# Kernel tuning notes

Measured on AMD Instinct MI355X. Metric: run time of the kernel, lower is better.

## Reference

```python
import jax, jax.numpy as jnp
import numpy as np

N = 100000
IN_C = 128
HID_C = 128
OUT_C = 128
E = 3200000


def setup_inputs() -> dict:
    key = jax.random.key(0)
    ks = jax.random.split(key, 8)
    x = jax.random.normal(ks[0], (N, IN_C), dtype=jnp.float32)
    edge_index = jax.random.randint(ks[1], (2, E), 0, N, dtype=jnp.int64)
    edge_weight = jnp.ones((E,), dtype=jnp.float32)
    s = 1.0 / np.sqrt(HID_C)
    W_conv = jax.random.uniform(ks[2], (HID_C, IN_C), jnp.float32, -s, s)
    b_conv = jnp.zeros((HID_C,), dtype=jnp.float32)
    W_fc = jax.random.uniform(ks[3], (HID_C, HID_C), jnp.float32, -s, s)
    b_fc = jax.random.uniform(ks[4], (HID_C,), jnp.float32, -s, s)
    W_fc2 = jax.random.uniform(ks[5], (OUT_C, HID_C), jnp.float32, -s, s)
    b_fc2 = jax.random.uniform(ks[6], (OUT_C,), jnp.float32, -s, s)
    return {"x": x, "edge_index": edge_index, "edge_weight": edge_weight,
            "W_conv": W_conv, "b_conv": b_conv, "W_fc": W_fc, "b_fc": b_fc,
            "W_fc2": W_fc2, "b_fc2": b_fc2}


def _gcn_conv(x, edge_index, edge_weight, W_conv, b_conv):
    n = x.shape[0]
    # add self-loops with weight 1 (PyG GCNConv default)
    loop = jnp.arange(n, dtype=edge_index.dtype)
    src = jnp.concatenate([edge_index[0], loop])
    dst = jnp.concatenate([edge_index[1], loop])
    ew = jnp.concatenate([edge_weight, jnp.ones((n,), dtype=edge_weight.dtype)])
    # symmetric normalization: deg^-1/2[src] * w * deg^-1/2[dst]
    deg = jax.ops.segment_sum(ew, dst, num_segments=n)
    dinv = jnp.where(deg > 0, jax.lax.rsqrt(jnp.where(deg > 0, deg, 1.0)), 0.0)
    norm = dinv[src] * ew * dinv[dst]  # [E+N]
    h = x @ W_conv.T                   # [N, hid], bias-free linear first
    msg = h[src] * norm[:, None]       # gather + scale
    agg = jax.ops.segment_sum(msg, dst, num_segments=n)  # scatter-add
    return agg + b_conv


def reference(x, edge_index, edge_weight, W_conv, b_conv, W_fc, b_fc, W_fc2, b_fc2):
    h = _gcn_conv(x, edge_index, edge_weight, W_conv, b_conv)
    h = jax.nn.relu(h)
    h = jax.nn.relu(h @ W_fc.T + b_fc)
    return h @ W_fc2.T + b_fc2
```

## Files before the change

kernel.cpp:

```cpp
#include <hip/hip_runtime.h>

typedef short bf16x8 __attribute__((ext_vector_type(8)));
typedef float f32x4 __attribute__((ext_vector_type(4)));

#define PS 64
#define PMAX 2048
#define CAPP 2432
#define NB 256

__device__ __forceinline__ unsigned short f2bf(float f) {
    unsigned int u = __float_as_uint(f);
    u = (u + 0x7FFFu + ((u >> 16) & 1u)) >> 16;
    return (unsigned short)u;
}
__device__ __forceinline__ float bf2f(unsigned short h) {
    return __uint_as_float(((unsigned int)h) << 16);
}

__global__ __launch_bounds__(1024) void scat_k(const int* __restrict__ ei,
                                               const float* __restrict__ ew,
                                               int* __restrict__ partCnt,
                                               int2* __restrict__ regions,
                                               int E, int P, int EPB) {
    __shared__ int cntl[PMAX];
    __shared__ int basel[PMAX];
    const int b = blockIdx.x, tid = threadIdx.x;
    for (int i = tid; i < P; i += 1024) cntl[i] = 0;
    __syncthreads();
    const int s = b * EPB, e = min(E, s + EPB);
    for (int i = s + tid; i < e; i += 1024)
        atomicAdd(&cntl[ei[E + i] >> 6], 1);
    __syncthreads();
    for (int p = tid; p < P; p += 1024) {
        int c = cntl[p];
        basel[p] = p * CAPP + (c ? atomicAdd(&partCnt[p], c) : 0);
        cntl[p] = 0;
    }
    __syncthreads();
    for (int i = s + tid; i < e; i += 1024) {
        int src = ei[i];
        int dst = ei[E + i];
        float w = ew[i];
        int p = dst >> 6, dl = dst & 63;
        int lidx = atomicAdd(&cntl[p], 1);
        int pos = basel[p] + lidx;
        if (pos < (p + 1) * CAPP)
            regions[pos] = make_int2(src | (dl << 24), __float_as_int(w));
    }
}

__global__ __launch_bounds__(256) void dgemm1_k(const float* __restrict__ x,
                                                const float* __restrict__ Wc,
                                                const int* __restrict__ partCnt,
                                                const int2* __restrict__ regions,
                                                float* __restrict__ dinv,
                                                unsigned short* __restrict__ h,
                                                int M, int P) {
    __shared__ __align__(16) unsigned short Wl[128 * 136];
    __shared__ float degl[256];
    const int tid = threadIdx.x;
    degl[tid] = 0.f;

#pragma unroll
    for (int i = 0; i < 16; ++i) {
        int e4 = i * 256 + tid;
        float4 v = ((const float4*)Wc)[e4];
        int e = e4 * 4, r = e >> 7, cc = e & 127;
        unsigned short* pp = &Wl[r * 136 + cc];
        pp[0] = f2bf(v.x); pp[1] = f2bf(v.y); pp[2] = f2bf(v.z); pp[3] = f2bf(v.w);
    }
    __syncthreads();

#pragma unroll
    for (int q = 0; q < 4; ++q) {
        int p = blockIdx.x * 4 + q;
        if (p < P) {
            const int cnt = min(partCnt[p], CAPP);
            const int2* reg = regions + (size_t)p * CAPP;
            for (int i = tid; i < cnt; i += 256) {
                int2 r = reg[i];
                atomicAdd(&degl[q * 64 + ((r.x >> 24) & 63)], __int_as_float(r.y));
            }
        }
    }
    __syncthreads();
    {
        int node = blockIdx.x * 256 + tid;
        float d = rsqrtf(1.0f + degl[tid]);
        if (node < M) dinv[node] = d;
        degl[tid] = d;
    }
    __syncthreads();

    const int wave = tid >> 6, lane = tid & 63;
    const int m = lane & 15, quad = lane >> 4;

#pragma unroll
    for (int t = 0; t < 4; ++t) {
        const int tileBase = blockIdx.x * 256 + t * 64;
        if (tileBase >= M) break;
        const int rowBase = tileBase + wave * 16;
        int arow = rowBase + m;
        int arowc = arow < M ? arow : (M - 1);

        bf16x8 afrag[4];
        const float* pa = x + (size_t)arowc * 128 + quad * 8;
#pragma unroll
        for (int kc = 0; kc < 4; ++kc) {
            float4 v0 = *(const float4*)(pa + kc * 32);
            float4 v1 = *(const float4*)(pa + kc * 32 + 4);
            bf16x8 f;
            f[0] = (short)f2bf(v0.x); f[1] = (short)f2bf(v0.y);
            f[2] = (short)f2bf(v0.z); f[3] = (short)f2bf(v0.w);
            f[4] = (short)f2bf(v1.x); f[5] = (short)f2bf(v1.y);
            f[6] = (short)f2bf(v1.z); f[7] = (short)f2bf(v1.w);
            afrag[kc] = f;
        }

        float dv[4];
#pragma unroll
        for (int r = 0; r < 4; ++r)
            dv[r] = degl[t * 64 + wave * 16 + quad * 4 + r];

#pragma unroll
        for (int nt = 0; nt < 8; ++nt) {
            f32x4 acc = {0.f, 0.f, 0.f, 0.f};
            const unsigned short* wb = &Wl[(nt * 16 + m) * 136 + quad * 8];
#pragma unroll
            for (int kc = 0; kc < 4; ++kc) {
                bf16x8 bfrag = *(const bf16x8*)(wb + kc * 32);
                acc = __builtin_amdgcn_mfma_f32_16x16x32_bf16(afrag[kc], bfrag, acc, 0, 0, 0);
            }
            const int col = nt * 16 + m;
#pragma unroll
            for (int r = 0; r < 4; ++r) {
                int row = rowBase + quad * 4 + r;
                if (row < M)
                    h[(size_t)row * 128 + col] = f2bf(acc[r] * dv[r]);
            }
        }
    }
}

__global__ __launch_bounds__(256) void aggF_k(const int* __restrict__ partCnt,
                                              const int2* __restrict__ regions,
                                              const unsigned short* __restrict__ h,
                                              const float* __restrict__ dinv,
                                              const float* __restrict__ bconv,
                                              unsigned short* __restrict__ h2, int N) {
    __shared__ __align__(16) int2 stag[CAPP];
    __shared__ int cl[PS];
    __shared__ int cstart[PS + 1];
    __shared__ int wcur[PS];
    const int p = blockIdx.x, tid = threadIdx.x;
    const int cnt = min(partCnt[p], CAPP);
    const int2* reg = regions + (size_t)p * CAPP;

    if (tid < PS) cl[tid] = 0;
    __syncthreads();
    for (int i = tid; i < cnt; i += 256)
        atomicAdd(&cl[(reg[i].x >> 24) & 63], 1);
    __syncthreads();
    if (tid < PS) {
        int cn = cl[tid];
        int v = cn;
#pragma unroll
        for (int off = 1; off < 64; off <<= 1) {
            int u = __shfl_up(v, off, 64);
            if (tid >= off) v += u;
        }
        cstart[tid + 1] = v;
        wcur[tid] = v - cn;
        if (tid == 0) cstart[0] = 0;
    }
    __syncthreads();
    for (int i = tid; i < cnt; i += 256) {
        int2 r = reg[i];
        int pos = atomicAdd(&wcur[(r.x >> 24) & 63], 1);
        stag[pos] = r;
    }
    __syncthreads();

    const int wave = tid >> 6, lane = tid & 63;
    const int g = lane >> 4;
    const int c8 = (lane & 15) * 8;
    for (int nl = wave; nl < PS; nl += 4) {
        int n = p * PS + nl;
        if (n >= N) continue;
        const int s = cstart[nl], e = cstart[nl + 1];
        float acc[8] = {0.f, 0.f, 0.f, 0.f, 0.f, 0.f, 0.f, 0.f};
        int j = s;
        const int efull = s + ((e - s) & ~15);
        for (; j < efull; j += 16) {
            int2 r0 = stag[j + g];
            int2 r1 = stag[j + 4 + g];
            int2 r2 = stag[j + 8 + g];
            int2 r3 = stag[j + 12 + g];
            float w0 = __int_as_float(r0.y), w1 = __int_as_float(r1.y);
            float w2 = __int_as_float(r2.y), w3 = __int_as_float(r3.y);
            int4 q0 = *(const int4*)(h + (((unsigned)r0.x & 0xFFFFFFu) << 7) + c8);
            int4 q1 = *(const int4*)(h + (((unsigned)r1.x & 0xFFFFFFu) << 7) + c8);
            int4 q2 = *(const int4*)(h + (((unsigned)r2.x & 0xFFFFFFu) << 7) + c8);
            int4 q3 = *(const int4*)(h + (((unsigned)r3.x & 0xFFFFFFu) << 7) + c8);
#pragma unroll
            for (int d = 0; d < 4; ++d) {
                unsigned ud = ((const unsigned*)&q0)[d];
                acc[2 * d]     += __uint_as_float(ud << 16) * w0;
                acc[2 * d + 1] += __uint_as_float(ud & 0xFFFF0000u) * w0;
            }
#pragma unroll
            for (int d = 0; d < 4; ++d) {
                unsigned ud = ((const unsigned*)&q1)[d];
                acc[2 * d]     += __uint_as_float(ud << 16) * w1;
                acc[2 * d + 1] += __uint_as_float(ud & 0xFFFF0000u) * w1;
            }
#pragma unroll
            for (int d = 0; d < 4; ++d) {
                unsigned ud = ((const unsigned*)&q2)[d];
                acc[2 * d]     += __uint_as_float(ud << 16) * w2;
                acc[2 * d + 1] += __uint_as_float(ud & 0xFFFF0000u) * w2;
            }
#pragma unroll
            for (int d = 0; d < 4; ++d) {
                unsigned ud = ((const unsigned*)&q3)[d];
                acc[2 * d]     += __uint_as_float(ud << 16) * w3;
                acc[2 * d + 1] += __uint_as_float(ud & 0xFFFF0000u) * w3;
            }
        }
        for (; j < e; j += 8) {
            int j0 = j + g, j1 = j + 4 + g;
            int2 r0 = stag[j0 < e ? j0 : s];
            int2 r1 = stag[j1 < e ? j1 : s];
            float w0 = (j0 < e) ? __int_as_float(r0.y) : 0.f;
            float w1 = (j1 < e) ? __int_as_float(r1.y) : 0.f;
            int4 q0 = *(const int4*)(h + (((unsigned)r0.x & 0xFFFFFFu) << 7) + c8);
            int4 q1 = *(const int4*)(h + (((unsigned)r1.x & 0xFFFFFFu) << 7) + c8);
#pragma unroll
            for (int d = 0; d < 4; ++d) {
                unsigned ud = ((const unsigned*)&q0)[d];
                acc[2 * d]     += __uint_as_float(ud << 16) * w0;
                acc[2 * d + 1] += __uint_as_float(ud & 0xFFFF0000u) * w0;
            }
#pragma unroll
            for (int d = 0; d < 4; ++d) {
                unsigned ud = ((const unsigned*)&q1)[d];
                acc[2 * d]     += __uint_as_float(ud << 16) * w1;
                acc[2 * d + 1] += __uint_as_float(ud & 0xFFFF0000u) * w1;
            }
        }
#pragma unroll
        for (int k = 0; k < 8; ++k) {
            float v = acc[k];
            v += __shfl_xor(v, 16, 64);
            v += __shfl_xor(v, 32, 64);
            acc[k] = v;
        }
        if (g == 0) {
            float di = dinv[n];
            int4 qs = *(const int4*)(h + ((unsigned)n << 7) + c8);
            float4 b0 = *(const float4*)(bconv + c8);
            float4 b1 = *(const float4*)(bconv + c8 + 4);
            float bb[8] = {b0.x, b0.y, b0.z, b0.w, b1.x, b1.y, b1.z, b1.w};
            bf16x8 o;
#pragma unroll
            for (int d = 0; d < 4; ++d) {
                unsigned ud = ((const unsigned*)&qs)[d];
                float h0 = __uint_as_float(ud << 16);
                float h1 = __uint_as_float(ud & 0xFFFF0000u);
                o[2 * d]     = (short)f2bf(fmaxf(di * (acc[2 * d] + h0) + bb[2 * d], 0.f));
                o[2 * d + 1] = (short)f2bf(fmaxf(di * (acc[2 * d + 1] + h1) + bb[2 * d + 1], 0.f));
            }
            *(bf16x8*)(h2 + (size_t)n * 128 + c8) = o;
        }
    }
}

__global__ __launch_bounds__(256) void gemm23_k(const unsigned short* __restrict__ h2,
                                                const float* __restrict__ Wf,
                                                const float* __restrict__ bfc,
                                                const float* __restrict__ W2,
                                                const float* __restrict__ b2,
                                                float* __restrict__ out, int M) {
    __shared__ __align__(16) unsigned short Wl[128 * 136];
    __shared__ __align__(16) unsigned short Tl[64 * 136];
    const int tid = threadIdx.x;

#pragma unroll
    for (int i = 0; i < 16; ++i) {
        int e4 = i * 256 + tid;
        float4 v = ((const float4*)Wf)[e4];
        int e = e4 * 4, r = e >> 7, cc = e & 127;
        unsigned short* pp = &Wl[r * 136 + cc];
        pp[0] = f2bf(v.x); pp[1] = f2bf(v.y); pp[2] = f2bf(v.z); pp[3] = f2bf(v.w);
    }
    __syncthreads();

    const int wave = tid >> 6, lane = tid & 63;
    const int m = lane & 15, quad = lane >> 4;
    const int rowBase = blockIdx.x * 64 + wave * 16;
    int arow = rowBase + m;
    int arowc = arow < M ? arow : (M - 1);

    bf16x8 afrag[4];
    {
        const unsigned short* pa = h2 + (size_t)arowc * 128 + quad * 8;
#pragma unroll
        for (int kc = 0; kc < 4; ++kc)
            afrag[kc] = *(const bf16x8*)(pa + kc * 32);
    }

#pragma unroll
    for (int nt = 0; nt < 8; ++nt) {
        f32x4 acc = {0.f, 0.f, 0.f, 0.f};
        const unsigned short* wb = &Wl[(nt * 16 + m) * 136 + quad * 8];
#pragma unroll
        for (int kc = 0; kc < 4; ++kc) {
            bf16x8 bfrag = *(const bf16x8*)(wb + kc * 32);
            acc = __builtin_amdgcn_mfma_f32_16x16x32_bf16(afrag[kc], bfrag, acc, 0, 0, 0);
        }
        const int col = nt * 16 + m;
        float bv = bfc[col];
#pragma unroll
        for (int r = 0; r < 4; ++r) {
            int rowl = wave * 16 + quad * 4 + r;
            Tl[rowl * 136 + col] = f2bf(fmaxf(acc[r] + bv, 0.f));
        }
    }
    __syncthreads();

#pragma unroll
    for (int i = 0; i < 16; ++i) {
        int e4 = i * 256 + tid;
        float4 v = ((const float4*)W2)[e4];
        int e = e4 * 4, r = e >> 7, cc = e & 127;
        unsigned short* pp = &Wl[r * 136 + cc];
        pp[0] = f2bf(v.x); pp[1] = f2bf(v.y); pp[2] = f2bf(v.z); pp[3] = f2bf(v.w);
    }
    __syncthreads();

    bf16x8 afrag2[4];
    {
        const unsigned short* pa = &Tl[(wave * 16 + m) * 136 + quad * 8];
#pragma unroll
        for (int kc = 0; kc < 4; ++kc)
            afrag2[kc] = *(const bf16x8*)(pa + kc * 32);
    }
#pragma unroll
    for (int nt = 0; nt < 8; ++nt) {
        f32x4 acc = {0.f, 0.f, 0.f, 0.f};
        const unsigned short* wb = &Wl[(nt * 16 + m) * 136 + quad * 8];
#pragma unroll
        for (int kc = 0; kc < 4; ++kc) {
            bf16x8 bfrag = *(const bf16x8*)(wb + kc * 32);
            acc = __builtin_amdgcn_mfma_f32_16x16x32_bf16(afrag2[kc], bfrag, acc, 0, 0, 0);
        }
        const int col = nt * 16 + m;
        float bv = b2[col];
#pragma unroll
        for (int r = 0; r < 4; ++r) {
            int row = rowBase + quad * 4 + r;
            if (row < M)
                out[(size_t)row * 128 + col] = acc[r] + bv;
        }
    }
}

extern "C" void kernel_launch(void* const* d_in, const int* in_sizes, int n_in,
                              void* d_out, int out_size, void* d_ws, size_t ws_size,
                              hipStream_t stream) {
    const float* x  = (const float*)d_in[0];
    const int* ei   = (const int*)d_in[1];
    const float* ew = (const float*)d_in[2];
    const float* Wc = (const float*)d_in[3];
    const float* bc = (const float*)d_in[4];
    const float* Wf = (const float*)d_in[5];
    const float* bf = (const float*)d_in[6];
    const float* W2 = (const float*)d_in[7];
    const float* b2 = (const float*)d_in[8];
    float* out = (float*)d_out;

    const int N = in_sizes[0] / 128;
    const int E = in_sizes[2];
    const int P = (N + PS - 1) / PS;

    auto align256 = [](size_t v) { return (v + 255) & ~(size_t)255; };
    char* ws = (char*)d_ws;
    size_t off = 0;
    float* dinv  = (float*)(ws + off); off += align256((size_t)N * 4);
    int* partCnt = (int*)(ws + off);   off += align256((size_t)P * 4);
    unsigned short* h  = (unsigned short*)(ws + off); off += (size_t)N * 256;
    unsigned short* h2 = (unsigned short*)(ws + off);

    int2* regions = (int2*)out;

    const int EPB = (E + NB - 1) / NB;

    hipMemsetAsync(partCnt, 0, (size_t)P * 4, stream);
    scat_k<<<NB, 1024, 0, stream>>>(ei, ew, partCnt, regions, E, P, EPB);
    dgemm1_k<<<(N + 255) / 256, 256, 0, stream>>>(x, Wc, partCnt, regions, dinv, h, N, P);
    aggF_k<<<P, 256, 0, stream>>>(partCnt, regions, h, dinv, bc, h2, N);
    gemm23_k<<<(N + 63) / 64, 256, 0, stream>>>(h2, Wf, bf, W2, b2, out, N);
}
```

Baseline: 384.2 us.

## Pre-convert weights to bf16, cache edge data in LDS, precompute node offsets, pipeline gathers

Adds a prologue kernel that converts all three weight matrices to bf16 once and zeroes the partition counters, replacing the memset. The GEMM kernels then read bf16 weights straight from global memory instead of staging converted copies in LDS. scat_k keeps dst and weight in LDS between its two passes so they are not reloaded from global memory. dgemm1_k now computes per-node offsets within each partition, which lets aggF_k skip its counting pass. aggF_k's gather loop is software-pipelined, prefetching the next 16 edges while the current chunk is accumulated. In exchange, scat_k uses about 100KB of LDS and may run at lower occupancy, and MFMA B operands now come from global or L2 rather than LDS.

```diff
diff --git a/kernel.cpp b/kernel.cpp
--- a/kernel.cpp
+++ b/kernel.cpp
@@ -7,14 +7,25 @@
 #define PMAX 2048
 #define CAPP 2432
 #define NB 256
+#define EPBC 12544
 
 __device__ __forceinline__ unsigned short f2bf(float f) {
     unsigned int u = __float_as_uint(f);
     u = (u + 0x7FFFu + ((u >> 16) & 1u)) >> 16;
     return (unsigned short)u;
 }
-__device__ __forceinline__ float bf2f(unsigned short h) {
-    return __uint_as_float(((unsigned int)h) << 16);
+
+__global__ __launch_bounds__(256) void pre_k(const float* __restrict__ Wc,
+                                             const float* __restrict__ Wf,
+                                             const float* __restrict__ W2,
+                                             unsigned short* __restrict__ Wb,
+                                             int* __restrict__ partCnt, int P) {
+    int i = blockIdx.x * 256 + threadIdx.x;
+    if (i < 3 * 16384) {
+        const float* src = (i < 16384) ? Wc : (i < 32768 ? Wf : W2);
+        Wb[i] = f2bf(src[i & 16383]);
+    }
+    if (i < P) partCnt[i] = 0;
 }
 
 __global__ __launch_bounds__(1024) void scat_k(const int* __restrict__ ei,
@@ -24,12 +35,19 @@
                                                int E, int P, int EPB) {
     __shared__ int cntl[PMAX];
     __shared__ int basel[PMAX];
+    __shared__ int dstl[EPBC];
+    __shared__ float ewl[EPBC];
     const int b = blockIdx.x, tid = threadIdx.x;
+    const bool useL = (EPB <= EPBC);
     for (int i = tid; i < P; i += 1024) cntl[i] = 0;
     __syncthreads();
     const int s = b * EPB, e = min(E, s + EPB);
-    for (int i = s + tid; i < e; i += 1024)
-        atomicAdd(&cntl[ei[E + i] >> 6], 1);
+    for (int i = s + tid; i < e; i += 1024) {
+        int dst = ei[E + i];
+        float w = ew[i];
+        if (useL) { dstl[i - s] = dst; ewl[i - s] = w; }
+        atomicAdd(&cntl[dst >> 6], 1);
+    }
     __syncthreads();
     for (int p = tid; p < P; p += 1024) {
         int c = cntl[p];
@@ -39,8 +57,8 @@
     __syncthreads();
     for (int i = s + tid; i < e; i += 1024) {
         int src = ei[i];
-        int dst = ei[E + i];
-        float w = ew[i];
+        int dst = useL ? dstl[i - s] : ei[E + i];
+        float w = useL ? ewl[i - s] : ew[i];
         int p = dst >> 6, dl = dst & 63;
         int lidx = atomicAdd(&cntl[p], 1);
         int pos = basel[p] + lidx;
@@ -50,25 +68,17 @@
 }
 
 __global__ __launch_bounds__(256) void dgemm1_k(const float* __restrict__ x,
-                                                const float* __restrict__ Wc,
+                                                const unsigned short* __restrict__ Wcb,
                                                 const int* __restrict__ partCnt,
                                                 const int2* __restrict__ regions,
                                                 float* __restrict__ dinv,
+                                                int* __restrict__ nodeOff,
                                                 unsigned short* __restrict__ h,
                                                 int M, int P) {
-    __shared__ __align__(16) unsigned short Wl[128 * 136];
     __shared__ float degl[256];
+    __shared__ int cl[256];
     const int tid = threadIdx.x;
-    degl[tid] = 0.f;
-
-#pragma unroll
-    for (int i = 0; i < 16; ++i) {
-        int e4 = i * 256 + tid;
-        float4 v = ((const float4*)Wc)[e4];
-        int e = e4 * 4, r = e >> 7, cc = e & 127;
-        unsigned short* pp = &Wl[r * 136 + cc];
-        pp[0] = f2bf(v.x); pp[1] = f2bf(v.y); pp[2] = f2bf(v.z); pp[3] = f2bf(v.w);
-    }
+    degl[tid] = 0.f; cl[tid] = 0;
     __syncthreads();
 
 #pragma unroll
@@ -79,15 +89,25 @@
             const int2* reg = regions + (size_t)p * CAPP;
             for (int i = tid; i < cnt; i += 256) {
                 int2 r = reg[i];
-                atomicAdd(&degl[q * 64 + ((r.x >> 24) & 63)], __int_as_float(r.y));
+                int dl = q * 64 + ((r.x >> 24) & 63);
+                atomicAdd(&cl[dl], 1);
+                atomicAdd(&degl[dl], __int_as_float(r.y));
             }
         }
     }
     __syncthreads();
     {
+        int lane = tid & 63;
+        int cn = cl[tid];
+        int v = cn;
+#pragma unroll
+        for (int off = 1; off < 64; off <<= 1) {
+            int u = __shfl_up(v, off, 64);
+            if (lane >= off) v += u;
+        }
         int node = blockIdx.x * 256 + tid;
         float d = rsqrtf(1.0f + degl[tid]);
-        if (node < M) dinv[node] = d;
+        if (node < M) { nodeOff[node] = v - cn; dinv[node] = d; }
         degl[tid] = d;
     }
     __syncthreads();
@@ -125,10 +145,9 @@
 #pragma unroll
         for (int nt = 0; nt < 8; ++nt) {
             f32x4 acc = {0.f, 0.f, 0.f, 0.f};
-            const unsigned short* wb = &Wl[(nt * 16 + m) * 136 + quad * 8];
 #pragma unroll
             for (int kc = 0; kc < 4; ++kc) {
-                bf16x8 bfrag = *(const bf16x8*)(wb + kc * 32);
+                bf16x8 bfrag = *(const bf16x8*)(Wcb + (nt * 16 + m) * 128 + kc * 32 + quad * 8);
                 acc = __builtin_amdgcn_mfma_f32_16x16x32_bf16(afrag[kc], bfrag, acc, 0, 0, 0);
             }
             const int col = nt * 16 + m;
@@ -143,35 +162,26 @@
 }
 
 __global__ __launch_bounds__(256) void aggF_k(const int* __restrict__ partCnt,
+                                              const int* __restrict__ nodeOff,
                                               const int2* __restrict__ regions,
                                               const unsigned short* __restrict__ h,
                                               const float* __restrict__ dinv,
                                               const float* __restrict__ bconv,
                                               unsigned short* __restrict__ h2, int N) {
     __shared__ __align__(16) int2 stag[CAPP];
-    __shared__ int cl[PS];
     __shared__ int cstart[PS + 1];
     __shared__ int wcur[PS];
     const int p = blockIdx.x, tid = threadIdx.x;
     const int cnt = min(partCnt[p], CAPP);
     const int2* reg = regions + (size_t)p * CAPP;
 
-    if (tid < PS) cl[tid] = 0;
-    __syncthreads();
-    for (int i = tid; i < cnt; i += 256)
-        atomicAdd(&cl[(reg[i].x >> 24) & 63], 1);
-    __syncthreads();
     if (tid < PS) {
-        int cn = cl[tid];
-        int v = cn;
-#pragma unroll
-        for (int off = 1; off < 64; off <<= 1) {
-            int u = __shfl_up(v, off, 64);
-            if (tid >= off) v += u;
-        }
-        cstart[tid + 1] = v;
-        wcur[tid] = v - cn;
-        if (tid == 0) cstart[0] = 0;
+        int node = p * PS + tid;
+        int o = (node < N) ? nodeOff[node] : cnt;
+        cstart[tid] = o;
+        wcur[tid] = o;
+    } else if (tid == PS) {
+        cstart[PS] = cnt;
     }
     __syncthreads();
     for (int i = tid; i < cnt; i += 256) {
@@ -187,67 +197,58 @@
     for (int nl = wave; nl < PS; nl += 4) {
         int n = p * PS + nl;
         if (n >= N) continue;
-        const int s = cstart[nl], e = cstart[nl + 1];
+        const int s0 = cstart[nl], e0 = cstart[nl + 1];
         float acc[8] = {0.f, 0.f, 0.f, 0.f, 0.f, 0.f, 0.f, 0.f};
-        int j = s;
-        const int efull = s + ((e - s) & ~15);
-        for (; j < efull; j += 16) {
-            int2 r0 = stag[j + g];
-            int2 r1 = stag[j + 4 + g];
-            int2 r2 = stag[j + 8 + g];
-            int2 r3 = stag[j + 12 + g];
-            float w0 = __int_as_float(r0.y), w1 = __int_as_float(r1.y);
-            float w2 = __int_as_float(r2.y), w3 = __int_as_float(r3.y);
-            int4 q0 = *(const int4*)(h + (((unsigned)r0.x & 0xFFFFFFu) << 7) + c8);
-            int4 q1 = *(const int4*)(h + (((unsigned)r1.x & 0xFFFFFFu) << 7) + c8);
-            int4 q2 = *(const int4*)(h + (((unsigned)r2.x & 0xFFFFFFu) << 7) + c8);
-            int4 q3 = *(const int4*)(h + (((unsigned)r3.x & 0xFFFFFFu) << 7) + c8);
+        const int chunks = (e0 - s0) >> 4;
+
+        int2 cr[4]; uint4 cq[4];
+        if (chunks > 0) {
+#pragma unroll
+            for (int t = 0; t < 4; ++t) cr[t] = stag[s0 + 4 * t + g];
+#pragma unroll
+            for (int t = 0; t < 4; ++t)
+                cq[t] = *(const uint4*)(h + (((unsigned)cr[t].x & 0xFFFFFFu) << 7) + c8);
+        }
+        for (int c = 0; c < chunks; ++c) {
+            int2 nr[4]; uint4 nq[4];
+            const bool more = (c + 1 < chunks);
+            if (more) {
+                int jb = s0 + 16 * (c + 1);
+#pragma unroll
+                for (int t = 0; t < 4; ++t) nr[t] = stag[jb + 4 * t + g];
+#pragma unroll
+                for (int t = 0; t < 4; ++t)
+                    nq[t] = *(const uint4*)(h + (((unsigned)nr[t].x & 0xFFFFFFu) << 7) + c8);
+            }
+#pragma unroll
+            for (int t = 0; t < 4; ++t) {
+                float w = __int_as_float(cr[t].y);
+#pragma unroll
+                for (int d = 0; d < 4; ++d) {
+                    unsigned ud = ((const unsigned*)&cq[t])[d];
+                    acc[2 * d]     += __uint_as_float(ud << 16) * w;
+                    acc[2 * d + 1] += __uint_as_float(ud & 0xFFFF0000u) * w;
+                }
+            }
+            if (more) {
+#pragma unroll
+                for (int t = 0; t < 4; ++t) { cr[t] = nr[t]; cq[t] = nq[t]; }
+            }
+        }
+        for (int j = s0 + (chunks << 4); j < e0; j += 4) {
+            int jj = j + g;
+            bool vld = jj < e0;
+            int2 r = stag[vld ? jj : s0];
+            float w = vld ? __int_as_float(r.y) : 0.f;
+            uint4 q = *(const uint4*)(h + (((unsigned)r.x & 0xFFFFFFu) << 7) + c8);
 #pragma unroll
             for (int d = 0; d < 4; ++d) {
-                unsigned ud = ((const unsigned*)&q0)[d];
-                acc[2 * d]     += __uint_as_float(ud << 16) * w0;
-                acc[2 * d + 1] += __uint_as_float(ud & 0xFFFF0000u) * w0;
-            }
-#pragma unroll
-            for (int d = 0; d < 4; ++d) {
-                unsigned ud = ((const unsigned*)&q1)[d];
-                acc[2 * d]     += __uint_as_float(ud << 16) * w1;
-                acc[2 * d + 1] += __uint_as_float(ud & 0xFFFF0000u) * w1;
-            }
-#pragma unroll
-            for (int d = 0; d < 4; ++d) {
-                unsigned ud = ((const unsigned*)&q2)[d];
-                acc[2 * d]     += __uint_as_float(ud << 16) * w2;
-                acc[2 * d + 1] += __uint_as_float(ud & 0xFFFF0000u) * w2;
-            }
-#pragma unroll
-            for (int d = 0; d < 4; ++d) {
-                unsigned ud = ((const unsigned*)&q3)[d];
-                acc[2 * d]     += __uint_as_float(ud << 16) * w3;
-                acc[2 * d + 1] += __uint_as_float(ud & 0xFFFF0000u) * w3;
-            }
-        }
-        for (; j < e; j += 8) {
-            int j0 = j + g, j1 = j + 4 + g;
-            int2 r0 = stag[j0 < e ? j0 : s];
-            int2 r1 = stag[j1 < e ? j1 : s];
-            float w0 = (j0 < e) ? __int_as_float(r0.y) : 0.f;
-            float w1 = (j1 < e) ? __int_as_float(r1.y) : 0.f;
-            int4 q0 = *(const int4*)(h + (((unsigned)r0.x & 0xFFFFFFu) << 7) + c8);
-            int4 q1 = *(const int4*)(h + (((unsigned)r1.x & 0xFFFFFFu) << 7) + c8);
-#pragma unroll
-            for (int d = 0; d < 4; ++d) {
-                unsigned ud = ((const unsigned*)&q0)[d];
-                acc[2 * d]     += __uint_as_float(ud << 16) * w0;
-                acc[2 * d + 1] += __uint_as_float(ud & 0xFFFF0000u) * w0;
-            }
-#pragma unroll
-            for (int d = 0; d < 4; ++d) {
-                unsigned ud = ((const unsigned*)&q1)[d];
-                acc[2 * d]     += __uint_as_float(ud << 16) * w1;
-                acc[2 * d + 1] += __uint_as_float(ud & 0xFFFF0000u) * w1;
-            }
-        }
+                unsigned ud = ((const unsigned*)&q)[d];
+                acc[2 * d]     += __uint_as_float(ud << 16) * w;
+                acc[2 * d + 1] += __uint_as_float(ud & 0xFFFF0000u) * w;
+            }
+        }
+
 #pragma unroll
         for (int k = 0; k < 8; ++k) {
             float v = acc[k];
@@ -257,7 +258,7 @@
         }
         if (g == 0) {
             float di = dinv[n];
-            int4 qs = *(const int4*)(h + ((unsigned)n << 7) + c8);
+            uint4 qs = *(const uint4*)(h + ((unsigned)n << 7) + c8);
             float4 b0 = *(const float4*)(bconv + c8);
             float4 b1 = *(const float4*)(bconv + c8 + 4);
             float bb[8] = {b0.x, b0.y, b0.z, b0.w, b1.x, b1.y, b1.z, b1.w};
@@ -276,25 +277,13 @@
 }
 
 __global__ __launch_bounds__(256) void gemm23_k(const unsigned short* __restrict__ h2,
-                                                const float* __restrict__ Wf,
+                                                const unsigned short* __restrict__ Wfb,
                                                 const float* __restrict__ bfc,
-                                                const float* __restrict__ W2,
+                                                const unsigned short* __restrict__ W2b,
                                                 const float* __restrict__ b2,
                                                 float* __restrict__ out, int M) {
-    __shared__ __align__(16) unsigned short Wl[128 * 136];
     __shared__ __align__(16) unsigned short Tl[64 * 136];
     const int tid = threadIdx.x;
-
-#pragma unroll
-    for (int i = 0; i < 16; ++i) {
-        int e4 = i * 256 + tid;
-        float4 v = ((const float4*)Wf)[e4];
-        int e = e4 * 4, r = e >> 7, cc = e & 127;
-        unsigned short* pp = &Wl[r * 136 + cc];
-        pp[0] = f2bf(v.x); pp[1] = f2bf(v.y); pp[2] = f2bf(v.z); pp[3] = f2bf(v.w);
-    }
-    __syncthreads();
-
     const int wave = tid >> 6, lane = tid & 63;
     const int m = lane & 15, quad = lane >> 4;
     const int rowBase = blockIdx.x * 64 + wave * 16;
@@ -312,10 +301,9 @@
 #pragma unroll
     for (int nt = 0; nt < 8; ++nt) {
         f32x4 acc = {0.f, 0.f, 0.f, 0.f};
-        const unsigned short* wb = &Wl[(nt * 16 + m) * 136 + quad * 8];
 #pragma unroll
         for (int kc = 0; kc < 4; ++kc) {
-            bf16x8 bfrag = *(const bf16x8*)(wb + kc * 32);
+            bf16x8 bfrag = *(const bf16x8*)(Wfb + (nt * 16 + m) * 128 + kc * 32 + quad * 8);
             acc = __builtin_amdgcn_mfma_f32_16x16x32_bf16(afrag[kc], bfrag, acc, 0, 0, 0);
         }
         const int col = nt * 16 + m;
@@ -328,16 +316,6 @@
     }
     __syncthreads();
 
-#pragma unroll
-    for (int i = 0; i < 16; ++i) {
-        int e4 = i * 256 + tid;
-        float4 v = ((const float4*)W2)[e4];
-        int e = e4 * 4, r = e >> 7, cc = e & 127;
-        unsigned short* pp = &Wl[r * 136 + cc];
-        pp[0] = f2bf(v.x); pp[1] = f2bf(v.y); pp[2] = f2bf(v.z); pp[3] = f2bf(v.w);
-    }
-    __syncthreads();
-
     bf16x8 afrag2[4];
     {
         const unsigned short* pa = &Tl[(wave * 16 + m) * 136 + quad * 8];
@@ -348,10 +326,9 @@
 #pragma unroll
     for (int nt = 0; nt < 8; ++nt) {
         f32x4 acc = {0.f, 0.f, 0.f, 0.f};
-        const unsigned short* wb = &Wl[(nt * 16 + m) * 136 + quad * 8];
 #pragma unroll
         for (int kc = 0; kc < 4; ++kc) {
-            bf16x8 bfrag = *(const bf16x8*)(wb + kc * 32);
+            bf16x8 bfrag = *(const bf16x8*)(W2b + (nt * 16 + m) * 128 + kc * 32 + quad * 8);
             acc = __builtin_amdgcn_mfma_f32_16x16x32_bf16(afrag2[kc], bfrag, acc, 0, 0, 0);
         }
         const int col = nt * 16 + m;
@@ -386,18 +363,24 @@
     auto align256 = [](size_t v) { return (v + 255) & ~(size_t)255; };
     char* ws = (char*)d_ws;
     size_t off = 0;
-    float* dinv  = (float*)(ws + off); off += align256((size_t)N * 4);
-    int* partCnt = (int*)(ws + off);   off += align256((size_t)P * 4);
+    float* dinv   = (float*)(ws + off); off += align256((size_t)N * 4);
+    int* nodeOff  = (int*)(ws + off);   off += align256((size_t)N * 4);
+    int* partCnt  = (int*)(ws + off);   off += align256((size_t)P * 4);
+    unsigned short* Wball = (unsigned short*)(ws + off); off += align256(3 * 16384 * 2);
     unsigned short* h  = (unsigned short*)(ws + off); off += (size_t)N * 256;
     unsigned short* h2 = (unsigned short*)(ws + off);
 
+    unsigned short* Wcb = Wball;
+    unsigned short* Wfb = Wball + 16384;
+    unsigned short* W2b = Wball + 32768;
+
     int2* regions = (int2*)out;
 
     const int EPB = (E + NB - 1) / NB;
 
-    hipMemsetAsync(partCnt, 0, (size_t)P * 4, stream);
+    pre_k<<<192, 256, 0, stream>>>(Wc, Wf, W2, Wball, partCnt, P);
     scat_k<<<NB, 1024, 0, stream>>>(ei, ew, partCnt, regions, E, P, EPB);
-    dgemm1_k<<<(N + 255) / 256, 256, 0, stream>>>(x, Wc, partCnt, regions, dinv, h, N, P);
-    aggF_k<<<P, 256, 0, stream>>>(partCnt, regions, h, dinv, bc, h2, N);
-    gemm23_k<<<(N + 63) / 64, 256, 0, stream>>>(h2, Wf, bf, W2, b2, out, N);
-}
+    dgemm1_k<<<(N + 255) / 256, 256, 0, stream>>>(x, Wcb, partCnt, regions, dinv, nodeOff, h, N, P);
+    aggF_k<<<P, 256, 0, stream>>>(partCnt, nodeOff, regions, h, dinv, bc, h2, N);
+    gemm23_k<<<(N + 63) / 64, 256, 0, stream>>>(h2, Wfb, bf, W2b, b2, out, N);
+}
```

New measurement: 414.8 us. 1.08x slower.
